# Performance work log

Hardware: AMD Instinct MI355X
Metric: run time of the kernel (lower is better)

## Reference

```python
import jax, jax.numpy as jnp
from jax import lax
import numpy as np

N_BASE = 4
STATE_LEN = 5
NUM_ROWS = N_BASE ** STATE_LEN        # 1024
ALPHA_LEN = N_BASE + 1                # 5, len('NACGT')
NEG = -1e30

# Sparse trellis gather indices (matches torch: cat([arange(NR)[:,None],
# arange(NR).repeat_interleave(n_base).reshape(n_base,-1).T], dim=1))
_r = np.arange(NUM_ROWS)
IDX = jnp.asarray(np.concatenate(
    [_r[:, None], np.repeat(_r, N_BASE).reshape(N_BASE, NUM_ROWS).T], axis=1))  # [NUM_ROWS, 5]


def _logZ_trellis(scores):
    # scores: [T, N, NUM_ROWS*(N_BASE+1)] -> logZ per batch [N]
    T, N, _ = scores.shape
    Ms = scores.reshape(T, N, NUM_ROWS, N_BASE + 1)
    alpha0 = jnp.zeros((N, NUM_ROWS), scores.dtype)  # Log semiring one = 0

    def step(alpha, M):
        # gather parent alphas via sparse idx, add transition scores, logsumexp
        return jax.nn.logsumexp(M + alpha[:, IDX], axis=-1), None

    alphaT, _ = lax.scan(step, alpha0, Ms)
    return jax.nn.logsumexp(alphaT, axis=-1)  # beta_T = 0


def _prepare_ctc_scores(scores, targets):
    T, N, C = scores.shape
    tgt = jnp.clip(targets - 1, 0)
    L = tgt.shape[1]
    n = L - (STATE_LEN - 1)
    stay_idx = sum(tgt[:, i:n + i] * (N_BASE ** (STATE_LEN - i - 1))
                   for i in range(STATE_LEN)) * ALPHA_LEN          # [N, n]
    move_idx = stay_idx[:, 1:] + tgt[:, :n - 1] + 1                # [N, n-1]
    stay = jnp.take_along_axis(scores, jnp.broadcast_to(stay_idx[None], (T, N, n)), axis=2)
    move = jnp.take_along_axis(scores, jnp.broadcast_to(move_idx[None], (T, N, n - 1)), axis=2)
    return stay, move


def _logZ_ctc(stay, move, lengths):
    # banded CTC-CRF alignment logZ. stay [T,N,n], move [T,N,n-1]
    T, N, n = stay.shape
    alpha0 = jnp.full((N, n), NEG, stay.dtype).at[:, 0].set(0.0)

    def step(alpha, sm):
        s, m = sm
        move_in = jnp.pad(alpha[:, :-1] + m, ((0, 0), (1, 0)), constant_values=NEG)
        return jnp.logaddexp(alpha + s, move_in), None

    alphaT, _ = lax.scan(step, alpha0, (stay, move))
    return alphaT[jnp.arange(N), lengths - 1]


def setup_inputs():
    key = jax.random.key(0)
    k1, k2 = jax.random.split(key)
    T, N, L = 500, 32, 400
    C = NUM_ROWS * ALPHA_LEN  # 5120
    scores = jax.random.normal(k1, (T, N, C), dtype=jnp.float32)
    targets = jax.random.randint(k2, (N, L), 1, N_BASE + 1, dtype=jnp.int32)
    target_lengths = jnp.full((N,), L, dtype=jnp.int32)
    return {"scores": scores, "targets": targets, "target_lengths": target_lengths}


def reference(scores, targets, target_lengths):
    # CTC_CRF.ctc_loss with normalise_scores=True, reduction='mean'
    T = scores.shape[0]
    logz_full = _logZ_trellis(scores)                 # [N]
    scores = scores - logz_full[None, :, None] / T    # normalise
    stay, move = _prepare_ctc_scores(scores, targets)
    logz = _logZ_ctc(stay, move, target_lengths + 1 - STATE_LEN)
    loss = -(logz / target_lengths)
    return loss.mean()
```

## Files before the change

kernel.cpp:

```cpp
#include <hip/hip_runtime.h>
#include <stdint.h>

#define TT 500
#define HT 250
#define NB 32
#define RS 1024
#define CD 5120
#define LT 400
#define NC 396
#define NEGF (-1e30f)
#define L2E 1.4426950408889634f
#define LN2f 0.6931471805599453f

#define SLAB_F CD
#define NRING 5
#define SMEM_FLOATS (NRING*SLAB_F + 2*RS)
#define SMEM_BYTES  (SMEM_FLOATS*4)

#define WS_AT 0
#define WS_BT (NB*RS)
#define WS_AC (2*NB*RS)
#define WS_BC (2*NB*RS + NB*NC)

__device__ __forceinline__ void stage5(const float* g, float* l, int lane) {
#pragma unroll
    for (int m = 0; m < 5; ++m) {
        __builtin_amdgcn_global_load_lds(
            (const __attribute__((address_space(1))) void*)(g + m*256 + lane*4),
            (__attribute__((address_space(3))) void*)(l + m*256),
            16, 0, 0);
    }
}

__device__ __forceinline__ float lse5(float t0, float t1, float t2, float t3, float t4) {
    float mx = fmaxf(fmaxf(fmaxf(t0,t1),t2), fmaxf(t3,t4));
    float e = exp2f(t0-mx)+exp2f(t1-mx)+exp2f(t2-mx)+exp2f(t3-mx)+exp2f(t4-mx);
    return mx + log2f(e);
}

#define PHASE_SYNC() do {                                  \
    __builtin_amdgcn_sched_barrier(0);                     \
    asm volatile("s_waitcnt vmcnt(15) lgkmcnt(0)");        \
    __builtin_amdgcn_s_barrier();                          \
    __builtin_amdgcn_sched_barrier(0);                     \
} while (0)

__device__ void trellis_fwd(const float* __restrict__ scores, float* __restrict__ ws,
                            int b, int tid, float* sm) {
    const int lane = tid & 63, w = tid >> 6;
    float* aping = sm + NRING*SLAB_F;
    float* apong = aping + RS;
    *(float4*)&aping[4*tid] = make_float4(0.f,0.f,0.f,0.f);
    __syncthreads();

    const size_t STP = (size_t)NB*CD;
    const float* gb = scores + (size_t)b*CD;
    const int woff = w*1280;
#pragma unroll
    for (int p = 0; p < 4; ++p)
        stage5(gb + (size_t)p*STP + woff, sm + p*SLAB_F + woff, lane);

    float ao[4] = {0.f,0.f,0.f,0.f};
    float* ar = aping; float* aw = apong;
    int t = 0;
    for (int it = 0; it < HT/NRING; ++it) {
#pragma unroll
        for (int k = 0; k < NRING; ++k) {
            PHASE_SYNC();
            int ts = t + 4; if (ts > HT-1) ts = HT-1;
            stage5(gb + (size_t)ts*STP + woff, sm + ((k+4)%NRING)*SLAB_F + woff, lane);
            const float4* S4 = (const float4*)(sm + k*SLAB_F + 20*tid);
            float4 r0=S4[0], r1=S4[1], r2=S4[2], r3=S4[3], r4=S4[4];
            float f[20] = {r0.x,r0.y,r0.z,r0.w, r1.x,r1.y,r1.z,r1.w,
                           r2.x,r2.y,r2.z,r2.w, r3.x,r3.y,r3.z,r3.w,
                           r4.x,r4.y,r4.z,r4.w};
            float p0 = ar[tid], p1 = ar[tid+256], p2 = ar[tid+512], p3 = ar[tid+768];
            float nw[4];
#pragma unroll
            for (int s = 0; s < 4; ++s) {
                nw[s] = lse5(fmaf(f[5*s+0],L2E,ao[s]), fmaf(f[5*s+1],L2E,p0),
                             fmaf(f[5*s+2],L2E,p1),   fmaf(f[5*s+3],L2E,p2),
                             fmaf(f[5*s+4],L2E,p3));
                ao[s] = nw[s];
            }
            *(float4*)&aw[4*tid] = make_float4(nw[0],nw[1],nw[2],nw[3]);
            float* tp_ = ar; ar = aw; aw = tp_;
            ++t;
        }
    }
    *(float4*)&ws[WS_AT + b*RS + 4*tid] = make_float4(ao[0],ao[1],ao[2],ao[3]);
}

__device__ void trellis_bwd(const float* __restrict__ scores, float* __restrict__ ws,
                            int b, int tid, float* sm) {
    const int lane = tid & 63, w = tid >> 6;
    float* bping = sm + NRING*SLAB_F;
    float* bpong = bping + RS;
    *(float4*)&bping[4*tid] = make_float4(0.f,0.f,0.f,0.f);
    __syncthreads();

    const size_t STP = (size_t)NB*CD;
    const float* gb = scores + (size_t)b*CD;
    const int woff = w*1280;
#pragma unroll
    for (int p = 0; p < 4; ++p)
        stage5(gb + (size_t)(TT-1-p)*STP + woff, sm + p*SLAB_F + woff, lane);

    float bo[4] = {0.f,0.f,0.f,0.f};
    float* br = bping; float* bw = bpong;
    int pp = 0;
    for (int it = 0; it < HT/NRING; ++it) {
#pragma unroll
        for (int k = 0; k < NRING; ++k) {
            PHASE_SYNC();
            int ps = pp + 4; if (ps > HT-1) ps = HT-1;
            stage5(gb + (size_t)(TT-1-ps)*STP + woff, sm + ((k+4)%NRING)*SLAB_F + woff, lane);
            float* slab = sm + k*SLAB_F;
            const float4* S4 = (const float4*)(slab + 20*tid);
            float4 r0=S4[0], r1=S4[1], r2=S4[2], r3=S4[3], r4=S4[4];
            float f[20] = {r0.x,r0.y,r0.z,r0.w, r1.x,r1.y,r1.z,r1.w,
                           r2.x,r2.y,r2.z,r2.w, r3.x,r3.y,r3.z,r3.w,
                           r4.x,r4.y,r4.z,r4.w};
            float st0 = slab[5*tid], st1 = slab[5*tid+1280],
                  st2 = slab[5*tid+2560], st3 = slab[5*tid+3840];
            float4 bc = *(const float4*)&br[4*tid];
            float nw[4];
            nw[0] = lse5(fmaf(st0,L2E,bo[0]), fmaf(f[1],L2E,bc.x), fmaf(f[6],L2E,bc.y),
                         fmaf(f[11],L2E,bc.z), fmaf(f[16],L2E,bc.w));
            nw[1] = lse5(fmaf(st1,L2E,bo[1]), fmaf(f[2],L2E,bc.x), fmaf(f[7],L2E,bc.y),
                         fmaf(f[12],L2E,bc.z), fmaf(f[17],L2E,bc.w));
            nw[2] = lse5(fmaf(st2,L2E,bo[2]), fmaf(f[3],L2E,bc.x), fmaf(f[8],L2E,bc.y),
                         fmaf(f[13],L2E,bc.z), fmaf(f[18],L2E,bc.w));
            nw[3] = lse5(fmaf(st3,L2E,bo[3]), fmaf(f[4],L2E,bc.x), fmaf(f[9],L2E,bc.y),
                         fmaf(f[14],L2E,bc.z), fmaf(f[19],L2E,bc.w));
            bo[0]=nw[0]; bo[1]=nw[1]; bo[2]=nw[2]; bo[3]=nw[3];
            bw[tid] = nw[0]; bw[tid+256] = nw[1]; bw[tid+512] = nw[2]; bw[tid+768] = nw[3];
            float* tp_ = br; br = bw; bw = tp_;
            ++pp;
        }
    }
    ws[WS_BT + b*RS + tid]       = bo[0];
    ws[WS_BT + b*RS + tid + 256] = bo[1];
    ws[WS_BT + b*RS + tid + 512] = bo[2];
    ws[WS_BT + b*RS + tid + 768] = bo[3];
}

__device__ __forceinline__ void ldc(const float* __restrict__ p,
                                    const int (&so)[7], const int (&mo)[7],
                                    float (&S)[7], float (&V)[7]) {
#pragma unroll
    for (int k = 0; k < 7; ++k) { S[k] = p[so[k]]; V[k] = p[mo[k]]; }
}

__device__ __forceinline__ void cstep(const float (&S)[7], const float (&V)[7],
                                      float (&ac)[7], int lane) {
    float prev = __shfl_up(ac[6], 1, 64);
    float nw[7];
#pragma unroll
    for (int k = 0; k < 7; ++k) {
        float left = k ? ac[k-1] : prev;
        float x = fmaf(S[k], L2E, ac[k]);
        float y = fmaf(V[k], L2E, left);
        if (k == 0) y = (lane == 0) ? NEGF : y;
        float m2 = fmaxf(x, y);
        float d  = fminf(x, y) - m2;
        nw[k] = m2 + log2f(1.0f + exp2f(d));
    }
#pragma unroll
    for (int k = 0; k < 7; ++k) ac[k] = nw[k];
}

__device__ __forceinline__ void cstep_b(const float (&S)[7], const float (&V)[7],
                                        float (&ac)[7], int lane) {
    float nxt = __shfl_down(ac[0], 1, 64);
    float nw[7];
#pragma unroll
    for (int k = 0; k < 7; ++k) {
        int gi = 7*lane + k;
        float bn = (k < 6) ? ac[k+1] : nxt;
        float x = fmaf(S[k], L2E, ac[k]);
        float y = fmaf(V[k], L2E, bn);
        y = (gi < NC-1) ? y : NEGF;
        float m2 = fmaxf(x, y);
        float d  = fminf(x, y) - m2;
        float r  = m2 + log2f(1.0f + exp2f(d));
        nw[k] = (gi < NC) ? r : NEGF;
    }
#pragma unroll
    for (int k = 0; k < 7; ++k) ac[k] = nw[k];
}

__device__ void build_tloc(const int* __restrict__ targets, int b, int lane, int (&tloc)[12]) {
#pragma unroll
    for (int j = 0; j < 12; ++j) {
        int gi = 7*lane - 1 + j;
        gi = gi < 0 ? 0 : (gi > LT-1 ? LT-1 : gi);
        int v = targets[b*LT + gi] - 1;
        tloc[j] = v < 0 ? 0 : v;
    }
}

__device__ void ctc_fwd(const float* __restrict__ scores, const int* __restrict__ targets,
                        float* __restrict__ ws, int b, int lane) {
    int tloc[12]; build_tloc(targets, b, lane, tloc);
    int so[7], mo[7];
#pragma unroll
    for (int k = 0; k < 7; ++k) {
        int gi = 7*lane + k;
        if (gi < NC) {
            int K = tloc[k+1];
            K = K*4 + tloc[k+2]; K = K*4 + tloc[k+3];
            K = K*4 + tloc[k+4]; K = K*4 + tloc[k+5];
            so[k] = K*5;
            mo[k] = (gi >= 1) ? (so[k] + tloc[k] + 1) : 0;
        } else { so[k] = 0; mo[k] = 0; }
    }
    float ac[7];
#pragma unroll
    for (int k = 0; k < 7; ++k) ac[k] = (7*lane + k == 0) ? 0.f : NEGF;

    const size_t STP = (size_t)NB*CD;
    const float* q0 = scores + (size_t)b*CD;
    const float* q1 = q0 + STP; const float* q2 = q0 + 2*STP; const float* q3 = q0 + 3*STP;
    float S0[7],V0[7],S1[7],V1[7],S2[7],V2[7],S3[7],V3[7];
    ldc(q0,so,mo,S0,V0); ldc(q1,so,mo,S1,V1); ldc(q2,so,mo,S2,V2); ldc(q3,so,mo,S3,V3);
    for (int t = 0; t < HT-2; t += 4) {
        cstep(S0,V0,ac,lane); if (t+4 < HT) { q0 += 4*STP; ldc(q0,so,mo,S0,V0); }
        cstep(S1,V1,ac,lane); if (t+5 < HT) { q1 += 4*STP; ldc(q1,so,mo,S1,V1); }
        cstep(S2,V2,ac,lane); if (t+6 < HT) { q2 += 4*STP; ldc(q2,so,mo,S2,V2); }
        cstep(S3,V3,ac,lane); if (t+7 < HT) { q3 += 4*STP; ldc(q3,so,mo,S3,V3); }
    }
    cstep(S0,V0,ac,lane);
    cstep(S1,V1,ac,lane);
#pragma unroll
    for (int k = 0; k < 7; ++k) {
        int gi = 7*lane + k;
        if (gi < NC) ws[WS_AC + b*NC + gi] = ac[k];
    }
}

__device__ void ctc_bwd(const float* __restrict__ scores, const int* __restrict__ targets,
                        const int* __restrict__ tlens, float* __restrict__ ws, int b, int lane) {
    int tloc[12]; build_tloc(targets, b, lane, tloc);
    int so[7], vo[7];
#pragma unroll
    for (int k = 0; k < 7; ++k) {
        int gi = 7*lane + k;
        if (gi < NC) {
            int K = tloc[k+1];
            K = K*4 + tloc[k+2]; K = K*4 + tloc[k+3];
            K = K*4 + tloc[k+4]; K = K*4 + tloc[k+5];
            so[k] = K*5;
            if (gi < NC-1) {
                int K2 = tloc[k+2];
                K2 = K2*4 + tloc[k+3]; K2 = K2*4 + tloc[k+4];
                K2 = K2*4 + tloc[k+5]; K2 = K2*4 + tloc[k+6];
                vo[k] = K2*5 + tloc[k+1] + 1;
            } else vo[k] = 0;
        } else { so[k] = 0; vo[k] = 0; }
    }
    int tl = tlens[b];
    float ac[7];
#pragma unroll
    for (int k = 0; k < 7; ++k) ac[k] = (7*lane + k == tl-5) ? 0.f : NEGF;

    const size_t STP = (size_t)NB*CD;
    const float* q0 = scores + ((size_t)(TT-1)*NB + b)*CD;
    const float* q1 = q0 - STP; const float* q2 = q0 - 2*STP; const float* q3 = q0 - 3*STP;
    float S0[7],V0[7],S1[7],V1[7],S2[7],V2[7],S3[7],V3[7];
    ldc(q0,so,vo,S0,V0); ldc(q1,so,vo,S1,V1); ldc(q2,so,vo,S2,V2); ldc(q3,so,vo,S3,V3);
    for (int p = 0; p < HT-2; p += 4) {
        cstep_b(S0,V0,ac,lane); if (p+4 < HT) { q0 -= 4*STP; ldc(q0,so,vo,S0,V0); }
        cstep_b(S1,V1,ac,lane); if (p+5 < HT) { q1 -= 4*STP; ldc(q1,so,vo,S1,V1); }
        cstep_b(S2,V2,ac,lane); if (p+6 < HT) { q2 -= 4*STP; ldc(q2,so,vo,S2,V2); }
        cstep_b(S3,V3,ac,lane); if (p+7 < HT) { q3 -= 4*STP; ldc(q3,so,vo,S3,V3); }
    }
    cstep_b(S0,V0,ac,lane);
    cstep_b(S1,V1,ac,lane);
#pragma unroll
    for (int k = 0; k < 7; ++k) {
        int gi = 7*lane + k;
        if (gi < NC) ws[WS_BC + b*NC + gi] = ac[k];
    }
}

extern "C" __global__ void __launch_bounds__(256, 1)
ctc_crf_main(const float* __restrict__ scores, const int* __restrict__ targets,
             const int* __restrict__ tlens, float* __restrict__ ws)
{
    extern __shared__ float sm[];
    const int blk = blockIdx.x, tid = threadIdx.x;
    if (blk < NB)            trellis_fwd(scores, ws, blk, tid, sm);
    else if (blk < 2*NB)     trellis_bwd(scores, ws, blk - NB, tid, sm);
    else if (blk < 3*NB)     { if (tid < 64) ctc_fwd(scores, targets, ws, blk - 2*NB, tid); }
    else                     { if (tid < 64) ctc_bwd(scores, targets, tlens, ws, blk - 3*NB, tid); }
}

extern "C" __global__ void __launch_bounds__(256, 1)
ctc_crf_combine(const float* __restrict__ ws, const int* __restrict__ tlens,
                float* __restrict__ out)
{
    const int b = blockIdx.x, tid = threadIdx.x, lane = tid & 63, w = tid >> 6;
    __shared__ float r1[4], r2[4];

    float4 a4 = *(const float4*)&ws[WS_AT + b*RS + 4*tid];
    float4 b4 = *(const float4*)&ws[WS_BT + b*RS + 4*tid];
    float v0 = a4.x+b4.x, v1 = a4.y+b4.y, v2 = a4.z+b4.z, v3 = a4.w+b4.w;
    float m = fmaxf(fmaxf(v0,v1), fmaxf(v2,v3));
#pragma unroll
    for (int o = 32; o >= 1; o >>= 1) m = fmaxf(m, __shfl_xor(m, o, 64));
    if (lane == 0) r1[w] = m;
    __syncthreads();
    float g = fmaxf(fmaxf(r1[0],r1[1]), fmaxf(r1[2],r1[3]));
    float e = exp2f(v0-g)+exp2f(v1-g)+exp2f(v2-g)+exp2f(v3-g);
#pragma unroll
    for (int o = 32; o >= 1; o >>= 1) e += __shfl_xor(e, o, 64);
    if (lane == 0) r2[w] = e;
    __syncthreads();
    float zfull = g + log2f(r2[0]+r2[1]+r2[2]+r2[3]);
    __syncthreads();

    float c0 = (tid < NC)     ? ws[WS_AC + b*NC + tid]       + ws[WS_BC + b*NC + tid]       : NEGF;
    float c1 = (tid+256 < NC) ? ws[WS_AC + b*NC + tid + 256] + ws[WS_BC + b*NC + tid + 256] : NEGF;
    float mc = fmaxf(c0, c1);
#pragma unroll
    for (int o = 32; o >= 1; o >>= 1) mc = fmaxf(mc, __shfl_xor(mc, o, 64));
    if (lane == 0) r1[w] = mc;
    __syncthreads();
    float gc = fmaxf(fmaxf(r1[0],r1[1]), fmaxf(r1[2],r1[3]));
    float ec = exp2f(c0-gc)+exp2f(c1-gc);
#pragma unroll
    for (int o = 32; o >= 1; o >>= 1) ec += __shfl_xor(ec, o, 64);
    if (lane == 0) r2[w] = ec;
    __syncthreads();
    if (tid == 0) {
        float zctc = gc + log2f(r2[0]+r2[1]+r2[2]+r2[3]);
        int tl = tlens[b];
        float loss_b = LN2f * (zfull - zctc) / (float)tl;
        atomicAdd(out, loss_b / (float)NB);
    }
}

extern "C" void kernel_launch(void* const* d_in, const int* in_sizes, int n_in,
                              void* d_out, int out_size, void* d_ws, size_t ws_size,
                              hipStream_t stream) {
    const float* scores  = (const float*)d_in[0];
    const int*   targets = (const int*)d_in[1];
    const int*   tlens   = (const int*)d_in[2];
    float* out = (float*)d_out;
    float* ws  = (float*)d_ws;

    hipFuncSetAttribute((const void*)ctc_crf_main,
                        hipFuncAttributeMaxDynamicSharedMemorySize, SMEM_BYTES);
    hipMemsetAsync(out, 0, sizeof(float), stream);
    ctc_crf_main<<<4*NB, 256, SMEM_BYTES, stream>>>(scores, targets, tlens, ws);
    ctc_crf_combine<<<NB, 256, 0, stream>>>(ws, tlens, out);
}
```

Measured before the change: 201.2 us.

## Fuse CTC recursion warp into trellis blocks sharing the LDS score ring

The CTC forward and backward recursions are moved into a fifth wavefront of the trellis forward and backward blocks, so they read stay/move scores from the shared-memory slabs already staged for the trellis instead of issuing their own scattered global loads. This halves the grid from 128 to 64 blocks. Staging is now spread over five waves, the ring grows to six slots with a deeper prefetch distance, and the next slab's LDS reads are software-pipelined one step ahead of the compute. The cost is a larger LDS footprint and the CTC warp being tied to the trellis barrier cadence.

```diff
diff --git a/kernel.cpp b/kernel.cpp
--- a/kernel.cpp
+++ b/kernel.cpp
@@ -13,7 +13,7 @@
 #define LN2f 0.6931471805599453f
 
 #define SLAB_F CD
-#define NRING 5
+#define NRING 6
 #define SMEM_FLOATS (NRING*SLAB_F + 2*RS)
 #define SMEM_BYTES  (SMEM_FLOATS*4)
 
@@ -22,134 +22,56 @@
 #define WS_AC (2*NB*RS)
 #define WS_BC (2*NB*RS + NB*NC)
 
-__device__ __forceinline__ void stage5(const float* g, float* l, int lane) {
-#pragma unroll
-    for (int m = 0; m < 5; ++m) {
+#define PHASE_SYNC() do {                                  \
+    __builtin_amdgcn_sched_barrier(0);                     \
+    asm volatile("s_waitcnt vmcnt(12) lgkmcnt(0)");        \
+    __builtin_amdgcn_s_barrier();                          \
+    __builtin_amdgcn_sched_barrier(0);                     \
+} while (0)
+
+struct S5 { float4 a, b, c, d, e; };
+
+__device__ __forceinline__ void stage4(const float* g, float* l, int lane) {
+#pragma unroll
+    for (int m = 0; m < 4; ++m)
         __builtin_amdgcn_global_load_lds(
             (const __attribute__((address_space(1))) void*)(g + m*256 + lane*4),
-            (__attribute__((address_space(3))) void*)(l + m*256),
-            16, 0, 0);
-    }
-}
-
-__device__ __forceinline__ float lse5(float t0, float t1, float t2, float t3, float t4) {
+            (__attribute__((address_space(3))) void*)(l + m*256), 16, 0, 0);
+}
+
+__device__ __forceinline__ void rd20(const float* p, S5& M) {
+    const float4* q = (const float4*)p;
+    M.a = q[0]; M.b = q[1]; M.c = q[2]; M.d = q[3]; M.e = q[4];
+}
+
+__device__ __forceinline__ float lse5(float t0,float t1,float t2,float t3,float t4){
     float mx = fmaxf(fmaxf(fmaxf(t0,t1),t2), fmaxf(t3,t4));
     float e = exp2f(t0-mx)+exp2f(t1-mx)+exp2f(t2-mx)+exp2f(t3-mx)+exp2f(t4-mx);
     return mx + log2f(e);
 }
 
-#define PHASE_SYNC() do {                                  \
-    __builtin_amdgcn_sched_barrier(0);                     \
-    asm volatile("s_waitcnt vmcnt(15) lgkmcnt(0)");        \
-    __builtin_amdgcn_s_barrier();                          \
-    __builtin_amdgcn_sched_barrier(0);                     \
-} while (0)
-
-__device__ void trellis_fwd(const float* __restrict__ scores, float* __restrict__ ws,
-                            int b, int tid, float* sm) {
-    const int lane = tid & 63, w = tid >> 6;
-    float* aping = sm + NRING*SLAB_F;
-    float* apong = aping + RS;
-    *(float4*)&aping[4*tid] = make_float4(0.f,0.f,0.f,0.f);
-    __syncthreads();
-
-    const size_t STP = (size_t)NB*CD;
-    const float* gb = scores + (size_t)b*CD;
-    const int woff = w*1280;
-#pragma unroll
-    for (int p = 0; p < 4; ++p)
-        stage5(gb + (size_t)p*STP + woff, sm + p*SLAB_F + woff, lane);
-
-    float ao[4] = {0.f,0.f,0.f,0.f};
-    float* ar = aping; float* aw = apong;
-    int t = 0;
-    for (int it = 0; it < HT/NRING; ++it) {
-#pragma unroll
-        for (int k = 0; k < NRING; ++k) {
-            PHASE_SYNC();
-            int ts = t + 4; if (ts > HT-1) ts = HT-1;
-            stage5(gb + (size_t)ts*STP + woff, sm + ((k+4)%NRING)*SLAB_F + woff, lane);
-            const float4* S4 = (const float4*)(sm + k*SLAB_F + 20*tid);
-            float4 r0=S4[0], r1=S4[1], r2=S4[2], r3=S4[3], r4=S4[4];
-            float f[20] = {r0.x,r0.y,r0.z,r0.w, r1.x,r1.y,r1.z,r1.w,
-                           r2.x,r2.y,r2.z,r2.w, r3.x,r3.y,r3.z,r3.w,
-                           r4.x,r4.y,r4.z,r4.w};
-            float p0 = ar[tid], p1 = ar[tid+256], p2 = ar[tid+512], p3 = ar[tid+768];
-            float nw[4];
-#pragma unroll
-            for (int s = 0; s < 4; ++s) {
-                nw[s] = lse5(fmaf(f[5*s+0],L2E,ao[s]), fmaf(f[5*s+1],L2E,p0),
-                             fmaf(f[5*s+2],L2E,p1),   fmaf(f[5*s+3],L2E,p2),
-                             fmaf(f[5*s+4],L2E,p3));
-                ao[s] = nw[s];
-            }
-            *(float4*)&aw[4*tid] = make_float4(nw[0],nw[1],nw[2],nw[3]);
-            float* tp_ = ar; ar = aw; aw = tp_;
-            ++t;
-        }
-    }
-    *(float4*)&ws[WS_AT + b*RS + 4*tid] = make_float4(ao[0],ao[1],ao[2],ao[3]);
-}
-
-__device__ void trellis_bwd(const float* __restrict__ scores, float* __restrict__ ws,
-                            int b, int tid, float* sm) {
-    const int lane = tid & 63, w = tid >> 6;
-    float* bping = sm + NRING*SLAB_F;
-    float* bpong = bping + RS;
-    *(float4*)&bping[4*tid] = make_float4(0.f,0.f,0.f,0.f);
-    __syncthreads();
-
-    const size_t STP = (size_t)NB*CD;
-    const float* gb = scores + (size_t)b*CD;
-    const int woff = w*1280;
-#pragma unroll
-    for (int p = 0; p < 4; ++p)
-        stage5(gb + (size_t)(TT-1-p)*STP + woff, sm + p*SLAB_F + woff, lane);
-
-    float bo[4] = {0.f,0.f,0.f,0.f};
-    float* br = bping; float* bw = bpong;
-    int pp = 0;
-    for (int it = 0; it < HT/NRING; ++it) {
-#pragma unroll
-        for (int k = 0; k < NRING; ++k) {
-            PHASE_SYNC();
-            int ps = pp + 4; if (ps > HT-1) ps = HT-1;
-            stage5(gb + (size_t)(TT-1-ps)*STP + woff, sm + ((k+4)%NRING)*SLAB_F + woff, lane);
-            float* slab = sm + k*SLAB_F;
-            const float4* S4 = (const float4*)(slab + 20*tid);
-            float4 r0=S4[0], r1=S4[1], r2=S4[2], r3=S4[3], r4=S4[4];
-            float f[20] = {r0.x,r0.y,r0.z,r0.w, r1.x,r1.y,r1.z,r1.w,
-                           r2.x,r2.y,r2.z,r2.w, r3.x,r3.y,r3.z,r3.w,
-                           r4.x,r4.y,r4.z,r4.w};
-            float st0 = slab[5*tid], st1 = slab[5*tid+1280],
-                  st2 = slab[5*tid+2560], st3 = slab[5*tid+3840];
-            float4 bc = *(const float4*)&br[4*tid];
-            float nw[4];
-            nw[0] = lse5(fmaf(st0,L2E,bo[0]), fmaf(f[1],L2E,bc.x), fmaf(f[6],L2E,bc.y),
-                         fmaf(f[11],L2E,bc.z), fmaf(f[16],L2E,bc.w));
-            nw[1] = lse5(fmaf(st1,L2E,bo[1]), fmaf(f[2],L2E,bc.x), fmaf(f[7],L2E,bc.y),
-                         fmaf(f[12],L2E,bc.z), fmaf(f[17],L2E,bc.w));
-            nw[2] = lse5(fmaf(st2,L2E,bo[2]), fmaf(f[3],L2E,bc.x), fmaf(f[8],L2E,bc.y),
-                         fmaf(f[13],L2E,bc.z), fmaf(f[18],L2E,bc.w));
-            nw[3] = lse5(fmaf(st3,L2E,bo[3]), fmaf(f[4],L2E,bc.x), fmaf(f[9],L2E,bc.y),
-                         fmaf(f[14],L2E,bc.z), fmaf(f[19],L2E,bc.w));
-            bo[0]=nw[0]; bo[1]=nw[1]; bo[2]=nw[2]; bo[3]=nw[3];
-            bw[tid] = nw[0]; bw[tid+256] = nw[1]; bw[tid+512] = nw[2]; bw[tid+768] = nw[3];
-            float* tp_ = br; br = bw; bw = tp_;
-            ++pp;
-        }
-    }
-    ws[WS_BT + b*RS + tid]       = bo[0];
-    ws[WS_BT + b*RS + tid + 256] = bo[1];
-    ws[WS_BT + b*RS + tid + 512] = bo[2];
-    ws[WS_BT + b*RS + tid + 768] = bo[3];
-}
-
-__device__ __forceinline__ void ldc(const float* __restrict__ p,
-                                    const int (&so)[7], const int (&mo)[7],
-                                    float (&S)[7], float (&V)[7]) {
-#pragma unroll
-    for (int k = 0; k < 7; ++k) { S[k] = p[so[k]]; V[k] = p[mo[k]]; }
+__device__ __forceinline__ void compute4(const S5& M, float (&ao)[4],
+                                         float p0, float p1, float p2, float p3) {
+    ao[0] = lse5(fmaf(M.a.x,L2E,ao[0]), fmaf(M.a.y,L2E,p0), fmaf(M.a.z,L2E,p1),
+                 fmaf(M.a.w,L2E,p2),   fmaf(M.b.x,L2E,p3));
+    ao[1] = lse5(fmaf(M.b.y,L2E,ao[1]), fmaf(M.b.z,L2E,p0), fmaf(M.b.w,L2E,p1),
+                 fmaf(M.c.x,L2E,p2),   fmaf(M.c.y,L2E,p3));
+    ao[2] = lse5(fmaf(M.c.z,L2E,ao[2]), fmaf(M.c.w,L2E,p0), fmaf(M.d.x,L2E,p1),
+                 fmaf(M.d.y,L2E,p2),   fmaf(M.d.z,L2E,p3));
+    ao[3] = lse5(fmaf(M.d.w,L2E,ao[3]), fmaf(M.e.x,L2E,p0), fmaf(M.e.y,L2E,p1),
+                 fmaf(M.e.z,L2E,p2),   fmaf(M.e.w,L2E,p3));
+}
+
+__device__ __forceinline__ void computeB(const S5& M, const float (&st)[4],
+                                         float (&bo)[4], float4 bc) {
+    bo[0] = lse5(fmaf(st[0],L2E,bo[0]), fmaf(M.a.y,L2E,bc.x), fmaf(M.b.z,L2E,bc.y),
+                 fmaf(M.c.w,L2E,bc.z), fmaf(M.e.x,L2E,bc.w));
+    bo[1] = lse5(fmaf(st[1],L2E,bo[1]), fmaf(M.a.z,L2E,bc.x), fmaf(M.b.w,L2E,bc.y),
+                 fmaf(M.d.x,L2E,bc.z), fmaf(M.e.y,L2E,bc.w));
+    bo[2] = lse5(fmaf(st[2],L2E,bo[2]), fmaf(M.a.w,L2E,bc.x), fmaf(M.c.x,L2E,bc.y),
+                 fmaf(M.d.y,L2E,bc.z), fmaf(M.e.z,L2E,bc.w));
+    bo[3] = lse5(fmaf(st[3],L2E,bo[3]), fmaf(M.b.x,L2E,bc.x), fmaf(M.c.y,L2E,bc.y),
+                 fmaf(M.d.z,L2E,bc.z), fmaf(M.e.w,L2E,bc.w));
 }
 
 __device__ __forceinline__ void cstep(const float (&S)[7], const float (&V)[7],
@@ -190,110 +112,151 @@
     for (int k = 0; k < 7; ++k) ac[k] = nw[k];
 }
 
-__device__ void build_tloc(const int* __restrict__ targets, int b, int lane, int (&tloc)[12]) {
-#pragma unroll
-    for (int j = 0; j < 12; ++j) {
-        int gi = 7*lane - 1 + j;
-        gi = gi < 0 ? 0 : (gi > LT-1 ? LT-1 : gi);
-        int v = targets[b*LT + gi] - 1;
-        tloc[j] = v < 0 ? 0 : v;
-    }
-}
-
-__device__ void ctc_fwd(const float* __restrict__ scores, const int* __restrict__ targets,
-                        float* __restrict__ ws, int b, int lane) {
-    int tloc[12]; build_tloc(targets, b, lane, tloc);
-    int so[7], mo[7];
-#pragma unroll
-    for (int k = 0; k < 7; ++k) {
-        int gi = 7*lane + k;
-        if (gi < NC) {
-            int K = tloc[k+1];
-            K = K*4 + tloc[k+2]; K = K*4 + tloc[k+3];
-            K = K*4 + tloc[k+4]; K = K*4 + tloc[k+5];
-            so[k] = K*5;
-            mo[k] = (gi >= 1) ? (so[k] + tloc[k] + 1) : 0;
-        } else { so[k] = 0; mo[k] = 0; }
-    }
-    float ac[7];
-#pragma unroll
-    for (int k = 0; k < 7; ++k) ac[k] = (7*lane + k == 0) ? 0.f : NEGF;
-
-    const size_t STP = (size_t)NB*CD;
-    const float* q0 = scores + (size_t)b*CD;
-    const float* q1 = q0 + STP; const float* q2 = q0 + 2*STP; const float* q3 = q0 + 3*STP;
-    float S0[7],V0[7],S1[7],V1[7],S2[7],V2[7],S3[7],V3[7];
-    ldc(q0,so,mo,S0,V0); ldc(q1,so,mo,S1,V1); ldc(q2,so,mo,S2,V2); ldc(q3,so,mo,S3,V3);
-    for (int t = 0; t < HT-2; t += 4) {
-        cstep(S0,V0,ac,lane); if (t+4 < HT) { q0 += 4*STP; ldc(q0,so,mo,S0,V0); }
-        cstep(S1,V1,ac,lane); if (t+5 < HT) { q1 += 4*STP; ldc(q1,so,mo,S1,V1); }
-        cstep(S2,V2,ac,lane); if (t+6 < HT) { q2 += 4*STP; ldc(q2,so,mo,S2,V2); }
-        cstep(S3,V3,ac,lane); if (t+7 < HT) { q3 += 4*STP; ldc(q3,so,mo,S3,V3); }
-    }
-    cstep(S0,V0,ac,lane);
-    cstep(S1,V1,ac,lane);
-#pragma unroll
-    for (int k = 0; k < 7; ++k) {
-        int gi = 7*lane + k;
-        if (gi < NC) ws[WS_AC + b*NC + gi] = ac[k];
-    }
-}
-
-__device__ void ctc_bwd(const float* __restrict__ scores, const int* __restrict__ targets,
-                        const int* __restrict__ tlens, float* __restrict__ ws, int b, int lane) {
-    int tloc[12]; build_tloc(targets, b, lane, tloc);
-    int so[7], vo[7];
-#pragma unroll
-    for (int k = 0; k < 7; ++k) {
-        int gi = 7*lane + k;
-        if (gi < NC) {
-            int K = tloc[k+1];
-            K = K*4 + tloc[k+2]; K = K*4 + tloc[k+3];
-            K = K*4 + tloc[k+4]; K = K*4 + tloc[k+5];
-            so[k] = K*5;
-            if (gi < NC-1) {
-                int K2 = tloc[k+2];
-                K2 = K2*4 + tloc[k+3]; K2 = K2*4 + tloc[k+4];
-                K2 = K2*4 + tloc[k+5]; K2 = K2*4 + tloc[k+6];
-                vo[k] = K2*5 + tloc[k+1] + 1;
-            } else vo[k] = 0;
-        } else { so[k] = 0; vo[k] = 0; }
-    }
-    int tl = tlens[b];
-    float ac[7];
-#pragma unroll
-    for (int k = 0; k < 7; ++k) ac[k] = (7*lane + k == tl-5) ? 0.f : NEGF;
-
-    const size_t STP = (size_t)NB*CD;
-    const float* q0 = scores + ((size_t)(TT-1)*NB + b)*CD;
-    const float* q1 = q0 - STP; const float* q2 = q0 - 2*STP; const float* q3 = q0 - 3*STP;
-    float S0[7],V0[7],S1[7],V1[7],S2[7],V2[7],S3[7],V3[7];
-    ldc(q0,so,vo,S0,V0); ldc(q1,so,vo,S1,V1); ldc(q2,so,vo,S2,V2); ldc(q3,so,vo,S3,V3);
-    for (int p = 0; p < HT-2; p += 4) {
-        cstep_b(S0,V0,ac,lane); if (p+4 < HT) { q0 -= 4*STP; ldc(q0,so,vo,S0,V0); }
-        cstep_b(S1,V1,ac,lane); if (p+5 < HT) { q1 -= 4*STP; ldc(q1,so,vo,S1,V1); }
-        cstep_b(S2,V2,ac,lane); if (p+6 < HT) { q2 -= 4*STP; ldc(q2,so,vo,S2,V2); }
-        cstep_b(S3,V3,ac,lane); if (p+7 < HT) { q3 -= 4*STP; ldc(q3,so,vo,S3,V3); }
-    }
-    cstep_b(S0,V0,ac,lane);
-    cstep_b(S1,V1,ac,lane);
-#pragma unroll
-    for (int k = 0; k < 7; ++k) {
-        int gi = 7*lane + k;
-        if (gi < NC) ws[WS_BC + b*NC + gi] = ac[k];
-    }
-}
-
-extern "C" __global__ void __launch_bounds__(256, 1)
+#define STAGE_ITER(j, slot) do {                                              \
+    int ts_ = (j) + 5; if (ts_ > HT-1) ts_ = HT-1;                            \
+    const float* src_ = gb + (size_t)(is_fwd ? ts_ : (TT-1-ts_)) * STP + woff;\
+    stage4(src_, sm + (slot)*SLAB_F + woff, lane);                            \
+} while (0)
+
+#define ROT6(x) do { x = (x == NRING-1) ? 0 : x + 1; } while (0)
+
+extern "C" __global__ void __launch_bounds__(320, 1)
 ctc_crf_main(const float* __restrict__ scores, const int* __restrict__ targets,
              const int* __restrict__ tlens, float* __restrict__ ws)
 {
     extern __shared__ float sm[];
-    const int blk = blockIdx.x, tid = threadIdx.x;
-    if (blk < NB)            trellis_fwd(scores, ws, blk, tid, sm);
-    else if (blk < 2*NB)     trellis_bwd(scores, ws, blk - NB, tid, sm);
-    else if (blk < 3*NB)     { if (tid < 64) ctc_fwd(scores, targets, ws, blk - 2*NB, tid); }
-    else                     { if (tid < 64) ctc_bwd(scores, targets, tlens, ws, blk - 3*NB, tid); }
+    const int tid = threadIdx.x, w = tid >> 6, lane = tid & 63;
+    const bool is_fwd = blockIdx.x < NB;
+    const int b = is_fwd ? (int)blockIdx.x : (int)blockIdx.x - NB;
+    const size_t STP = (size_t)NB * CD;
+    const float* gb = scores + (size_t)b * CD;
+    float* A0 = sm + NRING*SLAB_F;
+    float* A1 = A0 + RS;
+    const int woff = w * 1024;
+
+    if (w < 4) *(float4*)&A0[4*tid] = make_float4(0.f,0.f,0.f,0.f);
+
+    int so[7], mo[7]; float ac[7];
+    if (w == 4) {
+        int tloc[12];
+#pragma unroll
+        for (int j = 0; j < 12; ++j) {
+            int gi = 7*lane - 1 + j;
+            gi = gi < 0 ? 0 : (gi > LT-1 ? LT-1 : gi);
+            int v = targets[b*LT + gi] - 1;
+            tloc[j] = v < 0 ? 0 : v;
+        }
+        int tl = tlens[b];
+#pragma unroll
+        for (int k = 0; k < 7; ++k) {
+            int gi = 7*lane + k;
+            if (gi < NC) {
+                int K = tloc[k+1];
+                K = K*4 + tloc[k+2]; K = K*4 + tloc[k+3];
+                K = K*4 + tloc[k+4]; K = K*4 + tloc[k+5];
+                so[k] = K*5;
+                if (is_fwd) {
+                    mo[k] = (gi >= 1) ? (so[k] + tloc[k] + 1) : 0;
+                } else if (gi < NC-1) {
+                    int K2 = tloc[k+2];
+                    K2 = K2*4 + tloc[k+3]; K2 = K2*4 + tloc[k+4];
+                    K2 = K2*4 + tloc[k+5]; K2 = K2*4 + tloc[k+6];
+                    mo[k] = K2*5 + tloc[k+1] + 1;
+                } else mo[k] = 0;
+            } else { so[k] = 0; mo[k] = 0; }
+            ac[k] = is_fwd ? ((gi == 0) ? 0.f : NEGF)
+                           : ((gi == tl-5) ? 0.f : NEGF);
+        }
+    }
+
+#pragma unroll
+    for (int p = 0; p < 5; ++p) {
+        const float* src = gb + (size_t)(is_fwd ? p : (TT-1-p)) * STP + woff;
+        stage4(src, sm + p*SLAB_F + woff, lane);
+    }
+    __syncthreads();
+
+    S5 Ma, Mb; float sta[4], stb[4]; float ao[4] = {0.f,0.f,0.f,0.f};
+    if (w < 4) {
+        rd20(sm + 20*tid, Ma);
+        if (!is_fwd) {
+            sta[0] = sm[5*tid];        sta[1] = sm[5*tid + 1280];
+            sta[2] = sm[5*tid + 2560]; sta[3] = sm[5*tid + 3840];
+        }
+    }
+
+    int s_rd = 1, s_st = 5, s_cur = 0;
+
+    for (int k = 0; k < HT; k += 2) {
+        PHASE_SYNC();
+        STAGE_ITER(k, s_st);
+        if (w < 4) {
+            if (is_fwd) {
+                float p0 = A0[tid], p1 = A0[tid+256], p2 = A0[tid+512], p3 = A0[tid+768];
+                rd20(sm + s_rd*SLAB_F + 20*tid, Mb);
+                compute4(Ma, ao, p0, p1, p2, p3);
+                *(float4*)&A1[4*tid] = make_float4(ao[0],ao[1],ao[2],ao[3]);
+            } else {
+                float4 bc = *(const float4*)&A0[4*tid];
+                const float* sl = sm + s_rd*SLAB_F;
+                rd20(sl + 20*tid, Mb);
+                stb[0] = sl[5*tid];        stb[1] = sl[5*tid + 1280];
+                stb[2] = sl[5*tid + 2560]; stb[3] = sl[5*tid + 3840];
+                computeB(Ma, sta, ao, bc);
+                A1[tid] = ao[0]; A1[tid+256] = ao[1]; A1[tid+512] = ao[2]; A1[tid+768] = ao[3];
+            }
+        } else {
+            const float* sl = sm + s_cur*SLAB_F;
+            float S[7], V[7];
+#pragma unroll
+            for (int kk = 0; kk < 7; ++kk) { S[kk] = sl[so[kk]]; V[kk] = sl[mo[kk]]; }
+            if (is_fwd) cstep(S, V, ac, lane); else cstep_b(S, V, ac, lane);
+        }
+        ROT6(s_rd); ROT6(s_st); ROT6(s_cur);
+
+        PHASE_SYNC();
+        STAGE_ITER(k+1, s_st);
+        if (w < 4) {
+            if (is_fwd) {
+                float p0 = A1[tid], p1 = A1[tid+256], p2 = A1[tid+512], p3 = A1[tid+768];
+                rd20(sm + s_rd*SLAB_F + 20*tid, Ma);
+                compute4(Mb, ao, p0, p1, p2, p3);
+                *(float4*)&A0[4*tid] = make_float4(ao[0],ao[1],ao[2],ao[3]);
+            } else {
+                float4 bc = *(const float4*)&A1[4*tid];
+                const float* sl = sm + s_rd*SLAB_F;
+                rd20(sl + 20*tid, Ma);
+                sta[0] = sl[5*tid];        sta[1] = sl[5*tid + 1280];
+                sta[2] = sl[5*tid + 2560]; sta[3] = sl[5*tid + 3840];
+                computeB(Mb, stb, ao, bc);
+                A0[tid] = ao[0]; A0[tid+256] = ao[1]; A0[tid+512] = ao[2]; A0[tid+768] = ao[3];
+            }
+        } else {
+            const float* sl = sm + s_cur*SLAB_F;
+            float S[7], V[7];
+#pragma unroll
+            for (int kk = 0; kk < 7; ++kk) { S[kk] = sl[so[kk]]; V[kk] = sl[mo[kk]]; }
+            if (is_fwd) cstep(S, V, ac, lane); else cstep_b(S, V, ac, lane);
+        }
+        ROT6(s_rd); ROT6(s_st); ROT6(s_cur);
+    }
+
+    if (w < 4) {
+        if (is_fwd) {
+            *(float4*)&ws[WS_AT + b*RS + 4*tid] = make_float4(ao[0],ao[1],ao[2],ao[3]);
+        } else {
+            ws[WS_BT + b*RS + tid]       = ao[0];
+            ws[WS_BT + b*RS + tid + 256] = ao[1];
+            ws[WS_BT + b*RS + tid + 512] = ao[2];
+            ws[WS_BT + b*RS + tid + 768] = ao[3];
+        }
+    } else {
+#pragma unroll
+        for (int k = 0; k < 7; ++k) {
+            int gi = 7*lane + k;
+            if (gi < NC) ws[(is_fwd ? WS_AC : WS_BC) + b*NC + gi] = ac[k];
+        }
+    }
 }
 
 extern "C" __global__ void __launch_bounds__(256, 1)
@@ -353,6 +316,6 @@
     hipFuncSetAttribute((const void*)ctc_crf_main,
                         hipFuncAttributeMaxDynamicSharedMemorySize, SMEM_BYTES);
     hipMemsetAsync(out, 0, sizeof(float), stream);
-    ctc_crf_main<<<4*NB, 256, SMEM_BYTES, stream>>>(scores, targets, tlens, ws);
+    ctc_crf_main<<<2*NB, 320, SMEM_BYTES, stream>>>(scores, targets, tlens, ws);
     ctc_crf_combine<<<NB, 256, 0, stream>>>(ws, tlens, out);
 }
```

New measurement: 342.1 us. +70.0%, slower.
